# Performance work log

Hardware: AMD Instinct MI355X
Metric: run time of the kernel (lower is better)

The kernel has to match this reference:

```python
import jax, jax.numpy as jnp
import numpy as np

IMG_H, IMG_W = 1024, 1024
STRIDES = (8, 16, 32, 64, 128)
NUM_CLASSES = 80
CONF_THR = 0.05
IOU_THR = 0.5
MAX_PER_CLASS = 100
MAX_DET = 100
K_CAND = 256  # candidates kept per class before greedy NMS (pre-sort cap)


def build_grids():
    gy, gx, gs = [], [], []
    for s in STRIDES:
        H, W = IMG_H // s, IMG_W // s
        h = jnp.arange(H, dtype=jnp.float32)
        w = jnp.arange(W, dtype=jnp.float32)
        gy_, gx_ = jnp.meshgrid(h, w)  # 'xy' indexing -> shape [W, H], matches tf.meshgrid
        gy.append(gy_.reshape(-1))
        gx.append(gx_.reshape(-1))
        gs.append(jnp.full((W * H,), float(s), dtype=jnp.float32))
    return jnp.concatenate(gy), jnp.concatenate(gx), jnp.concatenate(gs)


def pairwise_iou(b):
    # b: [K,4] as (y1, x1, y2, x2)
    y1, x1, y2, x2 = b[:, 0], b[:, 1], b[:, 2], b[:, 3]
    area = (y2 - y1) * (x2 - x1)
    ih = jnp.maximum(jnp.minimum(y2[:, None], y2[None, :]) - jnp.maximum(y1[:, None], y1[None, :]), 0.0)
    iw = jnp.maximum(jnp.minimum(x2[:, None], x2[None, :]) - jnp.maximum(x1[:, None], x1[None, :]), 0.0)
    inter = ih * iw
    union = area[:, None] + area[None, :] - inter
    return inter / jnp.maximum(union, 1e-8)


def nms_one_class(boxes, scores):
    # boxes [N,4], scores [N] -> (sel_boxes [MAX_PER_CLASS,4], sel_scores [MAX_PER_CLASS])
    top_s, idx = jax.lax.top_k(scores, K_CAND)
    cand = boxes[idx]                       # [K,4]
    valid = top_s > CONF_THR
    iou = jax.lax.stop_gradient(pairwise_iou(cand))  # suppression mask is non-differentiable
    rng = jnp.arange(K_CAND)

    def body(i, keep):
        sup = (iou[i] > IOU_THR) & (rng > i) & keep[i]
        return keep & ~sup

    keep = jax.lax.fori_loop(0, K_CAND, body, valid)
    kept = jnp.where(keep, top_s, 0.0)
    sel_s, sel_i = jax.lax.top_k(kept, MAX_PER_CLASS)
    return cand[sel_i], sel_s


def combined_nms(boxes, scores):
    # per image: boxes [N,4] shared across classes, scores [N,C]
    cls_boxes, cls_scores = jax.vmap(nms_one_class, in_axes=(None, 1))(boxes, scores)
    C = scores.shape[1]
    cls_labels = jnp.broadcast_to(jnp.arange(C, dtype=jnp.float32)[:, None], cls_scores.shape)
    flat_s = cls_scores.reshape(-1)
    flat_b = cls_boxes.reshape(-1, 4)
    flat_l = cls_labels.reshape(-1)
    fin_s, fin_i = jax.lax.top_k(flat_s, MAX_DET)
    fin_b = flat_b[fin_i] * (fin_s > 0.0)[:, None].astype(flat_b.dtype)  # zero pad boxes like TF
    fin_l = flat_l[fin_i]
    return fin_b, fin_l, fin_s


def decode(pred_regs, pred_ctrs, pred_clfs):
    gy, gx, gs = build_grids()
    gy, gx, gs = gy[:, None], gx[:, None], gs[:, None]     # [N,1]
    score = pred_clfs * pred_ctrs                           # [B,N,C]
    x1 = gx - pred_regs[..., 0:1]
    x2 = gx + pred_regs[..., 1:2]
    y1 = gy - pred_regs[..., 2:3]
    y2 = gy + pred_regs[..., 3:4]
    bbox = jnp.concatenate([y1, x1, y2, x2], axis=-1) * gs  # [B,N,4] in image coords
    return jax.vmap(combined_nms)(bbox, score)


def setup_inputs() -> dict:
    key = jax.random.key(0)
    k1, k2, k3 = jax.random.split(key, 3)
    N = sum((IMG_H // s) * (IMG_W // s) for s in STRIDES)  # 21824
    B = 16
    return {
        "pred_regs": jax.random.uniform(k1, (B, N, 4), jnp.float32),
        "pred_ctrs": jax.random.uniform(k2, (B, N, 1), jnp.float32),
        "pred_clfs": jax.random.uniform(k3, (B, N, NUM_CLASSES), jnp.float32),
    }


def reference(pred_regs, pred_ctrs, pred_clfs):
    # returns (final_bboxes [B,100,4], final_labels [B,100] float, final_scores [B,100])
    return decode(pred_regs, pred_ctrs, pred_clfs)
```

## Files before the change

### kernel.cpp

```cpp
#include <hip/hip_runtime.h>
#include <stdint.h>

#pragma clang fp contract(off)

namespace {
constexpr int kN = 21824;
constexpr int kB = 16;
constexpr int kC = 80;
constexpr int kK = 256;
constexpr int kMaxPC = 100;
constexpr int kMaxDet = 100;
constexpr int kBins1 = 2048;
constexpr int kCap = 1536;
constexpr int kQCap = 320;
constexpr int kSortN = 512;
constexpr int kRows = kB * kC;
constexpr int kTiles = kN / 64;
constexpr int kTPB = 6;
constexpr int kGScan = (kTiles + kTPB - 1) / kTPB;
constexpr int kLCap = 48;
constexpr float kThr = 0.72f;
}

__device__ __forceinline__ uint64_t make_key(float s, int n) {
  return ((uint64_t)__float_as_uint(s) << 16) | (uint32_t)(0xFFFF - n);
}

__device__ uint32_t block_scan_incl(uint32_t val) {
  __shared__ uint32_t wsum[4];
  int lane = threadIdx.x & 63;
  int wave = threadIdx.x >> 6;
  for (int d = 1; d < 64; d <<= 1) {
    uint32_t t = __shfl_up(val, (unsigned)d, 64);
    if (lane >= d) val += t;
  }
  if (lane == 63) wsum[wave] = val;
  __syncthreads();
  uint32_t off = 0;
  for (int w = 0; w < wave; ++w) off += wsum[w];
  __syncthreads();
  return val + off;
}

struct RegSrc {
  uint64_t k[6];
  int cnt;
  template <class F> __device__ void each(F f) const {
    #pragma unroll
    for (int j = 0; j < 6; ++j)
      if (j < cnt) f(k[j]);
  }
};
struct ColSrc {
  const float* cl;
  const float* ct;
  template <class F> __device__ void each(F f) const {
    for (int n = threadIdx.x; n < kN; n += 256)
      f(make_key(cl[(size_t)n * kC] * ct[n], n));
  }
};
struct ArrSrc {
  const float* s;
  int count;
  template <class F> __device__ void each(F f) const {
    for (int i = threadIdx.x; i < count; i += 256) f(make_key(s[i], i));
  }
};

template <class Src>
__device__ int refine_gather(const Src& src, int K, int cap,
                             uint32_t* hist, uint64_t* cbuf) {
  __shared__ int sel_bin;
  __shared__ uint32_t sel_hd, sel_above, qcnt;
  int tid = threadIdx.x;

  for (int i = tid; i < kBins1; i += 256) hist[i] = 0;
  __syncthreads();
  src.each([&](uint64_t k) { atomicAdd(&hist[(uint32_t)(k >> 37)], 1u); });
  __syncthreads();
  uint32_t krem = (uint32_t)K;
  {
    uint32_t bl[8], v = 0;
    int base = kBins1 - 1 - 8 * tid;
    for (int j = 0; j < 8; ++j) { bl[j] = hist[base - j]; v += bl[j]; }
    uint32_t S = block_scan_incl(v);
    if (S >= krem && (S - v) < krem) {
      uint32_t cum = S - v;
      for (int j = 0; j < 8; ++j) {
        cum += bl[j];
        if (cum >= krem) { sel_bin = base - j; sel_hd = bl[j]; sel_above = cum - bl[j]; break; }
      }
    }
    __syncthreads();
  }
  uint64_t prefix = (uint64_t)sel_bin;
  krem = (uint32_t)K - sel_above;
  uint32_t Sge = ((uint32_t)K - krem) + sel_hd;
  int shift = 37;
  __syncthreads();

  while (Sge > (uint32_t)cap) {
    int w = (shift > 8) ? 8 : shift;
    int ns = shift - w, bins = 1 << w, hs = shift;
    for (int i = tid; i < bins; i += 256) hist[i] = 0;
    __syncthreads();
    uint64_t pfx = prefix;
    src.each([&](uint64_t k) {
      if ((k >> hs) == pfx)
        atomicAdd(&hist[(uint32_t)(k >> ns) & (bins - 1)], 1u);
    });
    __syncthreads();
    uint32_t v = (tid < bins) ? hist[bins - 1 - tid] : 0;
    uint32_t S = block_scan_incl(v);
    if (v && S >= krem && (S - v) < krem) {
      sel_bin = bins - 1 - tid; sel_hd = v; sel_above = S - v;
    }
    __syncthreads();
    prefix = (prefix << w) | (uint32_t)sel_bin;
    krem -= sel_above;
    Sge = ((uint32_t)K - krem) + sel_hd;
    shift = ns;
    __syncthreads();
  }

  uint64_t L = prefix << shift;
  if (tid == 0) qcnt = 0;
  __syncthreads();
  src.each([&](uint64_t k) {
    if (k >= L) {
      uint32_t p = atomicAdd(&qcnt, 1u);
      if (p < (uint32_t)cap) cbuf[p] = k;
    }
  });
  __syncthreads();
  int Scnt = (int)qcnt;
  return Scnt > cap ? cap : Scnt;
}

__global__ __launch_bounds__(256) void score_scan_kernel(
    const float* __restrict__ clfs, const float* __restrict__ ctrs,
    uint32_t* __restrict__ gcnt, uint64_t* __restrict__ glist) {
  int b = blockIdx.y;
  int t0 = blockIdx.x * kTPB;
  int t1 = t0 + kTPB; if (t1 > kTiles) t1 = kTiles;
  int nbase = t0 * 64;
  int nanch = (t1 - t0) * 64;

  __shared__ uint64_t lbuf[kC][kLCap + 1];
  __shared__ uint32_t lcnt[kC];
  __shared__ uint32_t gbase[kC];
  __shared__ float ct[kTPB * 64];
  int tid = threadIdx.x;
  for (int i = tid; i < kC; i += 256) lcnt[i] = 0;
  for (int i = tid; i < nanch; i += 256) ct[i] = ctrs[(size_t)b * kN + nbase + i];
  __syncthreads();

  const float4* src = (const float4*)(clfs + ((size_t)b * kN + nbase) * kC);
  int n4 = nanch * (kC / 4);
  float4 v = (tid < n4) ? src[tid] : float4{0, 0, 0, 0};
  for (int e = tid; e < n4; e += 256) {
    int en = e + 256;
    float4 vn = (en < n4) ? src[en] : float4{0, 0, 0, 0};
    int a = e / 20;
    int c0 = (e % 20) * 4;
    float cv = ct[a];
    int n = nbase + a;
    float sv[4] = {v.x * cv, v.y * cv, v.z * cv, v.w * cv};
    #pragma unroll
    for (int j = 0; j < 4; ++j) {
      if (sv[j] > kThr) {
        int c = c0 + j;
        uint32_t p = atomicAdd(&lcnt[c], 1u);
        if (p < kLCap) lbuf[c][p] = make_key(sv[j], n);
      }
    }
    v = vn;
  }
  __syncthreads();

  if (tid < kC) {
    uint32_t m = lcnt[tid];
    int row = b * kC + tid;
    if (m > kLCap) {
      atomicAdd(&gcnt[row], (uint32_t)(kCap + 1));
      gbase[tid] = 0xFFFFFFFFu;
    } else {
      gbase[tid] = m ? atomicAdd(&gcnt[row], m) : 0u;
    }
  }
  __syncthreads();

  int lane = tid & 63, wave = tid >> 6;
  for (int c = wave * 20; c < wave * 20 + 20; ++c) {
    uint32_t m = lcnt[c];
    uint32_t base = gbase[c];
    if (base == 0xFFFFFFFFu || m == 0) continue;
    if (m > kLCap) m = kLCap;
    int row = b * kC + c;
    for (uint32_t i = lane; i < m; i += 64) {
      uint32_t p = base + i;
      if (p < kCap) glist[(size_t)row * kCap + p] = lbuf[c][i];
    }
  }
}

__device__ __forceinline__ uint64_t iou_bit(const float4& A, float aA,
                                            const float4& Bx, float aB) {
  float yy1 = fmaxf(A.x, Bx.x);
  float yy2 = fminf(A.z, Bx.z);
  float xx1 = fmaxf(A.y, Bx.y);
  float xx2 = fminf(A.w, Bx.w);
  float ih = fmaxf(yy2 - yy1, 0.0f);
  float iw = fmaxf(xx2 - xx1, 0.0f);
  float inter = ih * iw;
  float un = (aB + aA) - inter;
  float unc = fmaxf(un, 1e-8f);
  return (uint64_t)(2.0f * inter > unc);
}

__global__ __launch_bounds__(256) void nms_class_kernel(
    const uint32_t* __restrict__ gcnt, const uint64_t* __restrict__ glist,
    const float* __restrict__ clfs, const float* __restrict__ ctrs,
    const float* __restrict__ regs,
    float* __restrict__ cls_boxes, float* __restrict__ cls_scores) {
  int row = blockIdx.x;
  int b = row / kC, c = row % kC;
  int tid = threadIdx.x;
  int lane = tid & 63, wave = tid >> 6;

  __shared__ union {
    uint32_t hist[kBins1];
    uint64_t sortb[kSortN];
    uint64_t supm[kK][4];
  } hu;
  __shared__ float4 boxf4[kK];
  __shared__ float barea[kK];
  __shared__ uint64_t kinit[4];
  __shared__ uint64_t kfin[4];

  uint32_t cnt = gcnt[row];
  int Scnt;
  if (cnt >= (uint32_t)kK && cnt <= (uint32_t)kCap) {
    RegSrc rs; rs.cnt = 0;
    const uint64_t* gl = glist + (size_t)row * kCap;
    #pragma unroll
    for (int j = 0; j < 6; ++j) {
      int i = tid + j * 256;
      if (i < (int)cnt) { rs.k[j] = gl[i]; rs.cnt = j + 1; }
    }
    Scnt = refine_gather(rs, kK, kSortN, hu.hist, hu.sortb);
  } else {
    ColSrc cs{clfs + (size_t)b * kN * kC + c, ctrs + (size_t)b * kN};
    Scnt = refine_gather(cs, kK, kSortN, hu.hist, hu.sortb);
  }

  for (int i = Scnt + tid; i < kSortN; i += 256) hu.sortb[i] = 0;
  __syncthreads();
  for (int k2 = 2; k2 <= kSortN; k2 <<= 1) {
    for (int j = k2 >> 1; j > 0; j >>= 1) {
      int lo = tid & (j - 1);
      int i = ((tid ^ lo) << 1) | lo;
      int p = i | j;
      uint64_t a = hu.sortb[i], bb = hu.sortb[p];
      bool sw = ((i & k2) != 0) ? (a > bb) : (a < bb);
      if (sw) { hu.sortb[i] = bb; hu.sortb[p] = a; }
      __syncthreads();
    }
  }
  uint64_t myk = hu.sortb[tid];
  __syncthreads();

  int n = 0xFFFF - (int)(myk & 0xFFFF);
  float sc_v = __uint_as_float((uint32_t)(myk >> 16));
  int off, hl;
  float sf;
  if (n < 16384)      { off = 0;     hl = 7; sf = 8.f;   }
  else if (n < 20480) { off = 16384; hl = 6; sf = 16.f;  }
  else if (n < 21504) { off = 20480; hl = 5; sf = 32.f;  }
  else if (n < 21760) { off = 21504; hl = 4; sf = 64.f;  }
  else                { off = 21760; hl = 3; sf = 128.f; }
  int kk = n - off;
  float gx = (float)(kk >> hl);
  float gy = (float)(kk & ((1 << hl) - 1));
  const float4 r = ((const float4*)regs)[(size_t)b * kN + n];
  float4 mybox;
  mybox.x = (gy - r.z) * sf;
  mybox.y = (gx - r.x) * sf;
  mybox.z = (gy + r.w) * sf;
  mybox.w = (gx + r.y) * sf;
  float my_a = (mybox.z - mybox.x) * (mybox.w - mybox.y);
  boxf4[tid] = mybox;
  barea[tid] = my_a;
  unsigned long long vm = __ballot(sc_v > 0.05f);
  if (lane == 0) kinit[wave] = vm;
  {
    uint64_t* sp = &hu.supm[0][0];
    #pragma unroll
    for (int q = 0; q < 4; ++q) sp[tid + q * 256] = 0;
  }
  __syncthreads();

  if (tid < 128) {
    int t = tid;
    uint64_t cur = 0;
    int jend = t + 127;
    for (int j = t + 1; j <= jend; ++j) {
      cur |= iou_bit(mybox, my_a, boxf4[j], barea[j]) << (j & 63);
      if ((j & 63) == 63) {
        if (cur) atomicOr((unsigned long long*)&hu.supm[t][j >> 6], cur);
        cur = 0;
      }
    }
    if (cur) atomicOr((unsigned long long*)&hu.supm[t][jend >> 6], cur);
  } else {
    int T = tid - 128;
    float4 bA = boxf4[T]; float aA = barea[T];
    uint64_t cur = 0;
    for (int j = T + 128; j <= 255; ++j) {
      cur |= iou_bit(bA, aA, boxf4[j], barea[j]) << (j & 63);
      if ((j & 63) == 63) {
        if (cur) atomicOr((unsigned long long*)&hu.supm[T][j >> 6], cur);
        cur = 0;
      }
    }
    if (T > 0) {
      int rB = 255 - T;
      float4 bB = boxf4[rB]; float aB = barea[rB];
      for (int j = 256 - T; j <= 255; ++j) {
        cur |= iou_bit(bB, aB, boxf4[j], barea[j]) << (j & 63);
        if ((j & 63) == 63) {
          if (cur) atomicOr((unsigned long long*)&hu.supm[rB][j >> 6], cur);
          cur = 0;
        }
      }
    }
  }
  __syncthreads();

  if (wave == 0) {
    uint64_t kw0 = kinit[0], kw1 = kinit[1], kw2 = kinit[2], kw3 = kinit[3];
    #define NMS_SECTION(W, KW)                                              \
      _Pragma("unroll")                                                     \
      for (int ch = 0; ch < 16; ++ch) {                                     \
        const ulonglong2* s0 = (const ulonglong2*)hu.supm[(W << 6) + ch * 4 + 0]; \
        const ulonglong2* s1 = (const ulonglong2*)hu.supm[(W << 6) + ch * 4 + 1]; \
        const ulonglong2* s2 = (const ulonglong2*)hu.supm[(W << 6) + ch * 4 + 2]; \
        const ulonglong2* s3 = (const ulonglong2*)hu.supm[(W << 6) + ch * 4 + 3]; \
        ulonglong2 aL = s0[0], aH = s0[1];                                  \
        ulonglong2 bL = s1[0], bH = s1[1];                                  \
        ulonglong2 cL = s2[0], cH = s2[1];                                  \
        ulonglong2 dL = s3[0], dH = s3[1];                                  \
        if ((KW >> (ch * 4 + 0)) & 1ull) { kw0 &= ~aL.x; kw1 &= ~aL.y; kw2 &= ~aH.x; kw3 &= ~aH.y; } \
        if ((KW >> (ch * 4 + 1)) & 1ull) { kw0 &= ~bL.x; kw1 &= ~bL.y; kw2 &= ~bH.x; kw3 &= ~bH.y; } \
        if ((KW >> (ch * 4 + 2)) & 1ull) { kw0 &= ~cL.x; kw1 &= ~cL.y; kw2 &= ~cH.x; kw3 &= ~cH.y; } \
        if ((KW >> (ch * 4 + 3)) & 1ull) { kw0 &= ~dL.x; kw1 &= ~dL.y; kw2 &= ~dH.x; kw3 &= ~dH.y; } \
      }
    NMS_SECTION(0, kw0)
    NMS_SECTION(1, kw1)
    NMS_SECTION(2, kw2)
    NMS_SECTION(3, kw3)
    #undef NMS_SECTION
    if (lane == 0) { kfin[0] = kw0; kfin[1] = kw1; kfin[2] = kw2; kfin[3] = kw3; }
  }
  __syncthreads();

  uint64_t kw0 = kfin[0], kw1 = kfin[1], kw2 = kfin[2], kw3 = kfin[3];
  uint64_t ww = (wave == 0) ? kw0 : (wave == 1) ? kw1 : (wave == 2) ? kw2 : kw3;
  bool keptf = (ww >> lane) & 1ull;
  int kept_total = (int)(__popcll(kw0) + __popcll(kw1) +
                         __popcll(kw2) + __popcll(kw3));
  int kept_before = (int)__popcll(ww & ((1ull << lane) - 1ull));
  if (wave > 0) kept_before += (int)__popcll(kw0);
  if (wave > 1) kept_before += (int)__popcll(kw1);
  if (wave > 2) kept_before += (int)__popcll(kw2);

  int rank2 = keptf ? kept_before : (kept_total + tid - kept_before);
  if (rank2 < kMaxPC) {
    float ks = keptf ? sc_v : 0.0f;
    size_t obase = ((size_t)row) * kMaxPC + rank2;
    cls_scores[obase] = ks;
    float* ob = cls_boxes + obase * 4;
    ob[0] = mybox.x; ob[1] = mybox.y; ob[2] = mybox.z; ob[3] = mybox.w;
  }
}

__global__ __launch_bounds__(256) void final_topk_kernel(
    const float* __restrict__ cls_scores, const float* __restrict__ cls_boxes,
    float* __restrict__ out) {
  int b = blockIdx.x;
  int tid = threadIdx.x;
  const int M = kC * kMaxPC;
  __shared__ uint32_t hist[kBins1];
  __shared__ uint64_t cbuf[kQCap];

  ArrSrc as{cls_scores + (size_t)b * M, M};
  int Scnt = refine_gather(as, kMaxDet, kQCap, hist, cbuf);

  for (int j = tid; j < Scnt; j += 256) {
    uint64_t myk = cbuf[j];
    int rank = 0;
    for (int i = 0; i < Scnt; ++i) rank += (cbuf[i] > myk);
    if (rank < kMaxDet) {
      float sv = __uint_as_float((uint32_t)(myk >> 16));
      int f = 0xFFFF - (int)(myk & 0xFFFF);
      int cls = f / 100;
      const float* bp = cls_boxes + ((size_t)b * M + f) * 4;
      float m = (sv > 0.0f) ? 1.0f : 0.0f;
      float* ob = out + ((size_t)b * kMaxDet + rank) * 4;
      ob[0] = bp[0] * m; ob[1] = bp[1] * m; ob[2] = bp[2] * m; ob[3] = bp[3] * m;
      out[(size_t)kB * kMaxDet * 4 + (size_t)b * kMaxDet + rank] = (float)cls;
      out[(size_t)kB * kMaxDet * 5 + (size_t)b * kMaxDet + rank] = sv;
    }
  }
}

extern "C" void kernel_launch(void* const* d_in, const int* in_sizes, int n_in,
                              void* d_out, int out_size, void* d_ws, size_t ws_size,
                              hipStream_t stream) {
  (void)in_sizes; (void)n_in; (void)out_size;
  const float* regs = (const float*)d_in[0];
  const float* ctrs = (const float*)d_in[1];
  const float* clfs = (const float*)d_in[2];
  float* out = (float*)d_out;

  const size_t glB  = (size_t)kRows * kCap * sizeof(uint64_t);
  const size_t cbB  = (size_t)kRows * kMaxPC * 4 * sizeof(float);
  const size_t csB  = (size_t)kRows * kMaxPC * sizeof(float);
  const size_t cntB = 8192;
  if (ws_size < glB + cbB + csB + cntB) return;

  char* p = (char*)d_ws;
  uint64_t* glist   = (uint64_t*)p; p += glB;
  float* cls_boxes  = (float*)p;    p += cbB;
  float* cls_scores = (float*)p;    p += csB;
  uint32_t* gcnt    = (uint32_t*)p;

  hipMemsetAsync(gcnt, 0, (size_t)kRows * sizeof(uint32_t), stream);
  score_scan_kernel<<<dim3(kGScan, kB), 256, 0, stream>>>(clfs, ctrs, gcnt, glist);
  nms_class_kernel<<<kRows, 256, 0, stream>>>(gcnt, glist, clfs, ctrs, regs,
                                              cls_boxes, cls_scores);
  final_topk_kernel<<<kB, 256, 0, stream>>>(cls_scores, cls_boxes, out);
}
```

Measured before the change: 285.6 us.

## Register-resident bitonic sort with wave shuffles and 32-bit IoU mask words

Each thread now holds two elements of the 512-key bitonic sort in registers. Compare-exchanges at strides below 128 use wave shuffles, so only the large-stride steps and the final step go through LDS with barriers, which removes most of the per-step __syncthreads. The IoU suppression mask is rebuilt with 32-bit words and 32-bit LDS atomicOr instead of 64-bit, and the mask-building loops are factored into one helper. The cost is more complex sort indexing and more atomic operations per row.

Measured after the change: 273.5 us. 4.3% less time.

```diff
diff --git a/kernel.cpp b/kernel.cpp
--- a/kernel.cpp
+++ b/kernel.cpp
@@ -204,18 +204,32 @@
   }
 }
 
-__device__ __forceinline__ uint64_t iou_bit(const float4& A, float aA,
-                                            const float4& Bx, float aB) {
-  float yy1 = fmaxf(A.x, Bx.x);
-  float yy2 = fminf(A.z, Bx.z);
-  float xx1 = fmaxf(A.y, Bx.y);
-  float xx2 = fminf(A.w, Bx.w);
-  float ih = fmaxf(yy2 - yy1, 0.0f);
-  float iw = fmaxf(xx2 - xx1, 0.0f);
-  float inter = ih * iw;
-  float un = (aB + aA) - inter;
-  float unc = fmaxf(un, 1e-8f);
-  return (uint64_t)(2.0f * inter > unc);
+__device__ __forceinline__ void iou_row_range(
+    const float4& A, float aA, const float4* boxes, const float* areas,
+    uint32_t (*sup)[8], int row, int j0, int j1 ) {
+  int j = j0;
+  while (j < j1) {
+    int wend = ((j >> 5) << 5) + 32;
+    if (wend > j1) wend = j1;
+    int w = j >> 5;
+    uint32_t cur = 0, m = 1u << (j & 31);
+    for (; j < wend; ++j) {
+      const float4 Bx = boxes[j];
+      float aB = areas[j];
+      float yy1 = fmaxf(A.x, Bx.x);
+      float yy2 = fminf(A.z, Bx.z);
+      float xx1 = fmaxf(A.y, Bx.y);
+      float xx2 = fminf(A.w, Bx.w);
+      float ih = fmaxf(yy2 - yy1, 0.0f);
+      float iw = fmaxf(xx2 - xx1, 0.0f);
+      float inter = ih * iw;
+      float un = (aB + aA) - inter;
+      float unc = fmaxf(un, 1e-8f);
+      cur |= (inter + inter > unc) ? m : 0u;
+      m += m;
+    }
+    if (cur) atomicOr(&sup[row][w], cur);
+  }
 }
 
 __global__ __launch_bounds__(256) void nms_class_kernel(
@@ -228,10 +242,10 @@
   int tid = threadIdx.x;
   int lane = tid & 63, wave = tid >> 6;
 
-  __shared__ union {
+  __shared__ union alignas(16) {
     uint32_t hist[kBins1];
     uint64_t sortb[kSortN];
-    uint64_t supm[kK][4];
+    uint32_t supm[kK][8];
   } hu;
   __shared__ float4 boxf4[kK];
   __shared__ float barea[kK];
@@ -256,17 +270,41 @@
 
   for (int i = Scnt + tid; i < kSortN; i += 256) hu.sortb[i] = 0;
   __syncthreads();
+  uint64_t e0 = hu.sortb[2 * tid], e1 = hu.sortb[2 * tid + 1];
+  #pragma unroll
   for (int k2 = 2; k2 <= kSortN; k2 <<= 1) {
-    for (int j = k2 >> 1; j > 0; j >>= 1) {
-      int lo = tid & (j - 1);
-      int i = ((tid ^ lo) << 1) | lo;
-      int p = i | j;
-      uint64_t a = hu.sortb[i], bb = hu.sortb[p];
-      bool sw = ((i & k2) != 0) ? (a > bb) : (a < bb);
-      if (sw) { hu.sortb[i] = bb; hu.sortb[p] = a; }
-      __syncthreads();
-    }
-  }
+    #pragma unroll
+    for (int j = k2 >> 1; j >= 2; j >>= 1) {
+      bool up = ((tid & (k2 >> 1)) == 0);
+      uint64_t p0, p1;
+      bool low;
+      if (j >= 128) {
+        __syncthreads();
+        hu.sortb[2 * tid] = e0; hu.sortb[2 * tid + 1] = e1;
+        __syncthreads();
+        int pi = (2 * tid) ^ j;
+        p0 = hu.sortb[pi]; p1 = hu.sortb[pi + 1];
+        low = ((tid & (j >> 1)) == 0);
+      } else {
+        int d = j >> 1;
+        p0 = (uint64_t)__shfl_xor((unsigned long long)e0, d, 64);
+        p1 = (uint64_t)__shfl_xor((unsigned long long)e1, d, 64);
+        low = ((tid & d) == 0);
+      }
+      bool keepMax = (up == low);
+      e0 = (keepMax == (e0 > p0)) ? e0 : p0;
+      e1 = (keepMax == (e1 > p1)) ? e1 : p1;
+    }
+    {
+      bool up = ((tid & (k2 >> 1)) == 0);
+      bool sw = up ? (e0 < e1) : (e0 > e1);
+      uint64_t t0 = sw ? e1 : e0, t1 = sw ? e0 : e1;
+      e0 = t0; e1 = t1;
+    }
+  }
+  __syncthreads();
+  hu.sortb[2 * tid] = e0; hu.sortb[2 * tid + 1] = e1;
+  __syncthreads();
   uint64_t myk = hu.sortb[tid];
   __syncthreads();
 
@@ -294,45 +332,22 @@
   unsigned long long vm = __ballot(sc_v > 0.05f);
   if (lane == 0) kinit[wave] = vm;
   {
-    uint64_t* sp = &hu.supm[0][0];
+    uint64_t* sp = (uint64_t*)&hu.supm[0][0];
     #pragma unroll
     for (int q = 0; q < 4; ++q) sp[tid + q * 256] = 0;
   }
   __syncthreads();
 
   if (tid < 128) {
-    int t = tid;
-    uint64_t cur = 0;
-    int jend = t + 127;
-    for (int j = t + 1; j <= jend; ++j) {
-      cur |= iou_bit(mybox, my_a, boxf4[j], barea[j]) << (j & 63);
-      if ((j & 63) == 63) {
-        if (cur) atomicOr((unsigned long long*)&hu.supm[t][j >> 6], cur);
-        cur = 0;
-      }
-    }
-    if (cur) atomicOr((unsigned long long*)&hu.supm[t][jend >> 6], cur);
+    iou_row_range(mybox, my_a, boxf4, barea, hu.supm, tid, tid + 1, tid + 128);
   } else {
     int T = tid - 128;
     float4 bA = boxf4[T]; float aA = barea[T];
-    uint64_t cur = 0;
-    for (int j = T + 128; j <= 255; ++j) {
-      cur |= iou_bit(bA, aA, boxf4[j], barea[j]) << (j & 63);
-      if ((j & 63) == 63) {
-        if (cur) atomicOr((unsigned long long*)&hu.supm[T][j >> 6], cur);
-        cur = 0;
-      }
-    }
+    iou_row_range(bA, aA, boxf4, barea, hu.supm, T, T + 128, 256);
     if (T > 0) {
       int rB = 255 - T;
       float4 bB = boxf4[rB]; float aB = barea[rB];
-      for (int j = 256 - T; j <= 255; ++j) {
-        cur |= iou_bit(bB, aB, boxf4[j], barea[j]) << (j & 63);
-        if ((j & 63) == 63) {
-          if (cur) atomicOr((unsigned long long*)&hu.supm[rB][j >> 6], cur);
-          cur = 0;
-        }
-      }
+      iou_row_range(bB, aB, boxf4, barea, hu.supm, rB, 256 - T, 256);
     }
   }
   __syncthreads();
```
